# Optimization experiments

Hardware: AMD Instinct MI355X
Metric: run time of the kernel (lower is better)

## Reference

```python
import jax, jax.numpy as jnp
import numpy as np
from math import sqrt

MEM_SIZE = 1024
MEM_DIM = 256


def setup_inputs() -> dict:
    key = jax.random.key(0)
    k1, k2, k3 = jax.random.split(key, 3)
    x = jax.random.normal(k1, (8, 256, 64, 64), dtype=jnp.float32)
    mask = jax.random.randint(k2, (8, 1, 64, 64), 0, 2).astype(jnp.bool_)
    mem = jax.random.normal(k3, (1, MEM_DIM, MEM_SIZE), dtype=jnp.float32)
    return {"x": x, "mask": mask, "mem": mem}


def reference(x, mask, mem):
    # masked-detach blend: x.detach() * ~mask + x * mask
    x = jnp.where(mask, x, jax.lax.stop_gradient(x))
    B, K, H, W = x.shape
    xf = x.reshape(B, K, H * W)            # (B, K, N)
    m = mem[0]                              # (K, M) with M = mem_size
    # logits = m_key @ x / sqrt(K)  -> (B, M, N)
    logits = jnp.einsum('km,bkn->bmn', m, xf) / sqrt(K)
    attn = jax.nn.softmax(logits, axis=1)   # softmax over memory axis
    # out = m @ attn -> (B, K, N)
    out = jnp.einsum('km,bmn->bkn', m, attn).reshape(B, K, H, W)
    return (out, logits)
```

## Files before the change

kernel.cpp:

```cpp
#include <hip/hip_runtime.h>
#include <stdint.h>


typedef __attribute__((ext_vector_type(8))) __bf16 bf16x8;
typedef __attribute__((ext_vector_type(4))) float f32x4;

#define BQ 8
#define KD 256
#define MD 1024
#define ND 4096
#define NT 64

__device__ __forceinline__ unsigned short bf16_rne(float f) {
    union { float f; uint32_t u; } c; c.f = f;
    uint32_t u = c.u;
    uint32_t r = (u + 0x7FFFu + ((u >> 16) & 1u)) >> 16;
    return (unsigned short)r;
}

__global__ void prep_mem(const float* __restrict__ mem,
                         unsigned short* __restrict__ mT,
                         unsigned short* __restrict__ mR) {
    const int k = blockIdx.x;
    const int t = threadIdx.x;
    float4 v = reinterpret_cast<const float4*>(mem + (size_t)k * MD)[t];
    unsigned short h0 = bf16_rne(v.x), h1 = bf16_rne(v.y),
                   h2 = bf16_rne(v.z), h3 = bf16_rne(v.w);
    reinterpret_cast<uint2*>(mR + (size_t)k * MD)[t] =
        make_uint2((uint32_t)h0 | ((uint32_t)h1 << 16),
                   (uint32_t)h2 | ((uint32_t)h3 << 16));
    const int mm = t * 4;
    mT[(size_t)(mm + 0) * KD + k] = h0;
    mT[(size_t)(mm + 1) * KD + k] = h1;
    mT[(size_t)(mm + 2) * KD + k] = h2;
    mT[(size_t)(mm + 3) * KD + k] = h3;
}

__global__ __launch_bounds__(1024, 4) void fused_attn_mem(
    const float* __restrict__ x,
    const unsigned short* __restrict__ mT,
    const unsigned short* __restrict__ mR,
    float* __restrict__ out,
    float* __restrict__ logits)
{
    extern __shared__ char lds[];
    float* red_max = (float*)(lds);
    float* red_sum = (float*)(lds + 4096);

    const int tid = threadIdx.x;
    const int w   = tid >> 6;
    const int l   = tid & 63;
    const int l15 = l & 15;
    const int l4  = l >> 4;

    const int bid = blockIdx.x;
    const int g   = bid & 7;
    const int j   = bid >> 3;
    const int strip = g * 8 + (j & 7);
    const int b     = j >> 3;
    const int n0    = strip * NT;

    {
        const float* xb = x + (size_t)b * KD * ND + n0;
        const int k  = tid >> 2;
        const int nh = (tid & 3) * 16;
        const f32x4* src = reinterpret_cast<const f32x4*>(xb + (size_t)k * ND + nh);
        f32x4 v0 = __builtin_nontemporal_load(src + 0);
        f32x4 v1 = __builtin_nontemporal_load(src + 1);
        f32x4 v2 = __builtin_nontemporal_load(src + 2);
        f32x4 v3 = __builtin_nontemporal_load(src + 3);
        float vals[16] = {v0[0], v0[1], v0[2], v0[3], v1[0], v1[1], v1[2], v1[3],
                          v2[0], v2[1], v2[2], v2[3], v3[0], v3[1], v3[2], v3[3]};
        #pragma unroll
        for (int jj = 0; jj < 16; ++jj) {
            const int n = nh + jj;
            const int off = n * 512 + (((k >> 3) ^ (n & 7)) << 4) + (k & 7) * 2;
            *(unsigned short*)(lds + off) = bf16_rne(vals[jj]);
        }
    }
    __syncthreads();

    f32x4 acc[4][4];
    #pragma unroll
    for (int rt = 0; rt < 4; ++rt)
        #pragma unroll
        for (int ct = 0; ct < 4; ++ct)
            acc[rt][ct] = (f32x4){0.f, 0.f, 0.f, 0.f};

    #pragma unroll
    for (int ks = 0; ks < 8; ++ks) {
        const int kk = ks * 32 + l4 * 8;
        bf16x8 bfr[4];
        #pragma unroll
        for (int ct = 0; ct < 4; ++ct) {
            const int n = ct * 16 + l15;
            const int off = n * 512 + (((kk >> 3) ^ (n & 7)) << 4);
            bfr[ct] = *(const bf16x8*)(lds + off);
        }
        #pragma unroll
        for (int rt = 0; rt < 4; ++rt) {
            const int row = w * 64 + rt * 16 + l15;
            const bf16x8 afr = *(const bf16x8*)(mT + (size_t)row * KD + kk);
            #pragma unroll
            for (int ct = 0; ct < 4; ++ct)
                acc[rt][ct] = __builtin_amdgcn_mfma_f32_16x16x32_bf16(afr, bfr[ct], acc[rt][ct], 0, 0, 0);
        }
    }

    float lmax[4] = {-3e38f, -3e38f, -3e38f, -3e38f};
    #pragma unroll
    for (int rt = 0; rt < 4; ++rt) {
        #pragma unroll
        for (int ct = 0; ct < 4; ++ct) {
            f32x4 v = acc[rt][ct] * 0.0625f;
            acc[rt][ct] = v;
            lmax[ct] = fmaxf(lmax[ct], fmaxf(fmaxf(v[0], v[1]), fmaxf(v[2], v[3])));
        }
    }

    {
        char* sw = lds + 32768 + w * 4608;
        float* lg = logits + (size_t)b * MD * ND + n0;
        #pragma unroll
        for (int rt = 0; rt < 4; ++rt) {
            #pragma unroll
            for (int ct = 0; ct < 4; ++ct) {
                const int n = ct * 16 + l15;
                #pragma unroll
                for (int r = 0; r < 4; ++r) {
                    const int mloc = l4 * 4 + r;
                    *(float*)(sw + mloc * 272 + n * 4) = acc[rt][ct][r];
                }
            }
            __asm__ volatile("s_waitcnt lgkmcnt(0)" ::: "memory");
            __builtin_amdgcn_sched_barrier(0);
            #pragma unroll
            for (int p = 0; p < 4; ++p) {
                const int mloc = p * 4 + l4;
                const f32x4 v = *(const f32x4*)(sw + mloc * 272 + l15 * 16);
                __builtin_nontemporal_store(v,
                    (f32x4*)(lg + (size_t)(w * 64 + rt * 16 + mloc) * ND + l15 * 4));
            }
            __asm__ volatile("s_waitcnt lgkmcnt(0)" ::: "memory");
            __builtin_amdgcn_sched_barrier(0);
        }
    }

    #pragma unroll
    for (int ct = 0; ct < 4; ++ct) {
        float m = lmax[ct];
        m = fmaxf(m, __shfl_xor(m, 16, 64));
        m = fmaxf(m, __shfl_xor(m, 32, 64));
        lmax[ct] = m;
    }
    __syncthreads();
    if (l < 16) {
        #pragma unroll
        for (int ct = 0; ct < 4; ++ct)
            red_max[(w * 4 + ct) * 16 + l] = lmax[ct];
    }
    __syncthreads();

    float cmax[4];
    #pragma unroll
    for (int ct = 0; ct < 4; ++ct) {
        float m = -3e38f;
        #pragma unroll
        for (int ww = 0; ww < 16; ++ww)
            m = fmaxf(m, red_max[(ww * 4 + ct) * 16 + l15]);
        cmax[ct] = m;
    }

    float lsum[4] = {0.f, 0.f, 0.f, 0.f};
    #pragma unroll
    for (int rt = 0; rt < 4; ++rt) {
        #pragma unroll
        for (int ct = 0; ct < 4; ++ct) {
            f32x4 v = acc[rt][ct];
            v[0] = __expf(v[0] - cmax[ct]);
            v[1] = __expf(v[1] - cmax[ct]);
            v[2] = __expf(v[2] - cmax[ct]);
            v[3] = __expf(v[3] - cmax[ct]);
            lsum[ct] += (v[0] + v[1]) + (v[2] + v[3]);
            acc[rt][ct] = v;
        }
    }
    #pragma unroll
    for (int ct = 0; ct < 4; ++ct) {
        float s = lsum[ct];
        s += __shfl_xor(s, 16, 64);
        s += __shfl_xor(s, 32, 64);
        lsum[ct] = s;
    }
    if (l < 16) {
        #pragma unroll
        for (int ct = 0; ct < 4; ++ct)
            red_sum[(w * 4 + ct) * 16 + l] = lsum[ct];
    }
    __syncthreads();

    float rs[4];
    #pragma unroll
    for (int ct = 0; ct < 4; ++ct) {
        float s = 0.f;
        #pragma unroll
        for (int ww = 0; ww < 16; ++ww)
            s += red_sum[(ww * 4 + ct) * 16 + l15];
        rs[ct] = 1.0f / s;
    }

    #pragma unroll
    for (int rt = 0; rt < 4; ++rt) {
        #pragma unroll
        for (int ct = 0; ct < 4; ++ct) {
            f32x4 v = acc[rt][ct];
            unsigned short h0 = bf16_rne(v[0] * rs[ct]);
            unsigned short h1 = bf16_rne(v[1] * rs[ct]);
            unsigned short h2 = bf16_rne(v[2] * rs[ct]);
            unsigned short h3 = bf16_rne(v[3] * rs[ct]);
            const int m0 = w * 64 + rt * 16 + l4 * 4;
            const int n  = ct * 16 + l15;
            const int off = 32768 + n * 2048 + (((m0 >> 3) ^ (n & 7)) << 4) + (m0 & 7) * 2;
            *(uint2*)(lds + off) = make_uint2((uint32_t)h0 | ((uint32_t)h1 << 16),
                                              (uint32_t)h2 | ((uint32_t)h3 << 16));
        }
    }
    __syncthreads();

    f32x4 acc2[4];
    #pragma unroll
    for (int ct = 0; ct < 4; ++ct)
        acc2[ct] = (f32x4){0.f, 0.f, 0.f, 0.f};

    const unsigned short* arow = mR + (size_t)(w * 16 + l15) * MD;
    #pragma unroll 4
    for (int ks = 0; ks < 32; ++ks) {
        const int mk = ks * 32 + l4 * 8;
        const bf16x8 a2 = *(const bf16x8*)(arow + mk);
        #pragma unroll
        for (int ct = 0; ct < 4; ++ct) {
            const int n = ct * 16 + l15;
            const int off = 32768 + n * 2048 + (((mk >> 3) ^ (n & 7)) << 4);
            const bf16x8 b2 = *(const bf16x8*)(lds + off);
            acc2[ct] = __builtin_amdgcn_mfma_f32_16x16x32_bf16(a2, b2, acc2[ct], 0, 0, 0);
        }
    }
    __syncthreads();

    {
        char* sw = lds + 32768 + w * 4608;
        float* ob = out + (size_t)b * KD * ND + n0;
        #pragma unroll
        for (int ct = 0; ct < 4; ++ct) {
            const int n = ct * 16 + l15;
            #pragma unroll
            for (int r = 0; r < 4; ++r) {
                const int rr = l4 * 4 + r;
                *(float*)(sw + rr * 272 + n * 4) = acc2[ct][r];
            }
        }
        __asm__ volatile("s_waitcnt lgkmcnt(0)" ::: "memory");
        __builtin_amdgcn_sched_barrier(0);
        #pragma unroll
        for (int p = 0; p < 4; ++p) {
            const int rr = p * 4 + l4;
            const f32x4 v = *(const f32x4*)(sw + rr * 272 + l15 * 16);
            __builtin_nontemporal_store(v,
                (f32x4*)(ob + (size_t)(w * 16 + rr) * ND + l15 * 4));
        }
    }
}

extern "C" void kernel_launch(void* const* d_in, const int* in_sizes, int n_in,
                              void* d_out, int out_size, void* d_ws, size_t ws_size,
                              hipStream_t stream) {
    (void)in_sizes; (void)n_in; (void)out_size; (void)ws_size;
    const float* x   = (const float*)d_in[0];
    const float* mem = (const float*)d_in[2];

    float* out    = (float*)d_out;
    float* logits = (float*)d_out + (size_t)BQ * KD * ND;

    unsigned short* mT = (unsigned short*)d_ws;
    unsigned short* mR = mT + (size_t)MD * KD;

    static int lds_attr_set = 0;
    if (!lds_attr_set) {
        (void)hipFuncSetAttribute(reinterpret_cast<const void*>(&fused_attn_mem),
                                  hipFuncAttributeMaxDynamicSharedMemorySize, 163840);
        lds_attr_set = 1;
    }

    prep_mem<<<dim3(256), dim3(256), 0, stream>>>(mem, mT, mR);
    fused_attn_mem<<<dim3(BQ * (ND / NT)), dim3(1024), 163840, stream>>>(x, mT, mR, out, logits);
}
```

Before: 113.4 us.

## Split fused attention into bf16 x-transpose, logits GEMM, and recompute tail kernels

```diff
diff --git a/kernel.cpp b/kernel.cpp
--- a/kernel.cpp
+++ b/kernel.cpp
@@ -4,6 +4,7 @@
 
 typedef __attribute__((ext_vector_type(8))) __bf16 bf16x8;
 typedef __attribute__((ext_vector_type(4))) float f32x4;
+typedef __attribute__((ext_vector_type(4))) unsigned int u32x4;
 
 #define BQ 8
 #define KD 256
@@ -36,6 +37,300 @@
     mT[(size_t)(mm + 3) * KD + k] = h3;
 }
 
+__global__ __launch_bounds__(1024, 4) void prep_xT(
+    const float* __restrict__ x, unsigned short* __restrict__ xT)
+{
+    __shared__ __align__(16) char lds[32768];
+    const int tid = threadIdx.x;
+    const int b  = blockIdx.x >> 6;
+    const int n0 = (blockIdx.x & 63) * 64;
+
+    {
+        const float* xb = x + (size_t)b * KD * ND + n0;
+        const int k  = tid >> 2;
+        const int nh = (tid & 3) * 16;
+        const f32x4* src = reinterpret_cast<const f32x4*>(xb + (size_t)k * ND + nh);
+        f32x4 v0 = __builtin_nontemporal_load(src + 0);
+        f32x4 v1 = __builtin_nontemporal_load(src + 1);
+        f32x4 v2 = __builtin_nontemporal_load(src + 2);
+        f32x4 v3 = __builtin_nontemporal_load(src + 3);
+        float vals[16] = {v0[0], v0[1], v0[2], v0[3], v1[0], v1[1], v1[2], v1[3],
+                          v2[0], v2[1], v2[2], v2[3], v3[0], v3[1], v3[2], v3[3]};
+        #pragma unroll
+        for (int jj = 0; jj < 16; ++jj) {
+            const int n = nh + jj;
+            const int off = n * 512 + (((k >> 3) ^ (n & 7)) << 4) + (k & 7) * 2;
+            *(unsigned short*)(lds + off) = bf16_rne(vals[jj]);
+        }
+    }
+    __syncthreads();
+    {
+        const int n = tid >> 4, seg = tid & 15;
+        u32x4 q0 = *(const u32x4*)(lds + n * 512 + (((2 * seg)     ^ (n & 7)) << 4));
+        u32x4 q1 = *(const u32x4*)(lds + n * 512 + (((2 * seg + 1) ^ (n & 7)) << 4));
+        u32x4* dst = (u32x4*)(xT + ((size_t)b * ND + n0 + n) * KD + seg * 16);
+        dst[0] = q0;
+        dst[1] = q1;
+    }
+}
+
+__global__ __launch_bounds__(512, 2) void k_logits(
+    const unsigned short* __restrict__ mT,
+    const unsigned short* __restrict__ xT,
+    float* __restrict__ logits)
+{
+    __shared__ __align__(16) float scr[8][4][256];
+
+    const int tid = threadIdx.x;
+    const int w   = tid >> 6;
+    const int l   = tid & 63;
+    const int l15 = l & 15;
+    const int l4  = l >> 4;
+
+    const int bid = blockIdx.x;
+    const int g   = bid & 7;
+    const int j   = bid >> 3;
+    const int c   = g * 8 + (j & 7);
+    const int mt  = j >> 3;
+    const int b   = c >> 3;
+    const int nt  = c & 7;
+
+    const int m0w = mt * 64 + (w >> 1) * 16;
+    const int n0w = nt * 512 + (w & 1) * 256;
+
+    f32x4 acc[16];
+    #pragma unroll
+    for (int ct = 0; ct < 16; ++ct) acc[ct] = (f32x4){0.f, 0.f, 0.f, 0.f};
+
+    #pragma unroll
+    for (int ks = 0; ks < 8; ++ks) {
+        const int kk = ks * 32 + l4 * 8;
+        const bf16x8 a = *(const bf16x8*)(mT + (size_t)(m0w + l15) * KD + kk);
+        #pragma unroll
+        for (int ct = 0; ct < 16; ++ct) {
+            const bf16x8 bf = *(const bf16x8*)(xT + ((size_t)b * ND + n0w + ct * 16 + l15) * KD + kk);
+            acc[ct] = __builtin_amdgcn_mfma_f32_16x16x32_bf16(a, bf, acc[ct], 0, 0, 0);
+        }
+    }
+    #pragma unroll
+    for (int ct = 0; ct < 16; ++ct) acc[ct] = acc[ct] * 0.0625f;
+
+    float* lgb = logits + (size_t)b * MD * ND;
+    #pragma unroll
+    for (int r = 0; r < 4; ++r) {
+        #pragma unroll
+        for (int ct = 0; ct < 16; ++ct) {
+            const int nn = ct * 16 + l15;
+            scr[w][l4][nn ^ (l4 << 3)] = acc[ct][r];
+        }
+        __asm__ volatile("s_waitcnt lgkmcnt(0)" ::: "memory");
+        __builtin_amdgcn_sched_barrier(0);
+        #pragma unroll
+        for (int s = 0; s < 4; ++s) {
+            const f32x4 v = *(const f32x4*)&scr[w][s][(4 * l) ^ (s << 3)];
+            __builtin_nontemporal_store(v,
+                (f32x4*)(lgb + (size_t)(m0w + s * 4 + r) * ND + n0w + 4 * l));
+        }
+        __asm__ volatile("s_waitcnt lgkmcnt(0)" ::: "memory");
+        __builtin_amdgcn_sched_barrier(0);
+    }
+}
+
+__global__ __launch_bounds__(1024, 4) void k_fused_tail(
+    const unsigned short* __restrict__ xT,
+    const unsigned short* __restrict__ mT,
+    const unsigned short* __restrict__ mR,
+    float* __restrict__ out)
+{
+    extern __shared__ char lds[];
+    float* red_max = (float*)(lds);
+    float* red_sum = (float*)(lds + 4096);
+
+    const int tid = threadIdx.x;
+    const int w   = tid >> 6;
+    const int l   = tid & 63;
+    const int l15 = l & 15;
+    const int l4  = l >> 4;
+
+    const int bid = blockIdx.x;
+    const int g   = bid & 7;
+    const int j   = bid >> 3;
+    const int strip = g * 8 + (j & 7);
+    const int b     = j >> 3;
+    const int n0    = strip * NT;
+
+    {
+        const int n = tid >> 4, seg = tid & 15;
+        const unsigned short* srow = xT + ((size_t)b * ND + n0 + n) * KD + seg * 16;
+        u32x4 q0 = *(const u32x4*)(srow);
+        u32x4 q1 = *(const u32x4*)(srow + 8);
+        *(u32x4*)(lds + n * 512 + (((2 * seg)     ^ (n & 7)) << 4)) = q0;
+        *(u32x4*)(lds + n * 512 + (((2 * seg + 1) ^ (n & 7)) << 4)) = q1;
+    }
+    __syncthreads();
+
+    f32x4 acc[4][4];
+    #pragma unroll
+    for (int rt = 0; rt < 4; ++rt)
+        #pragma unroll
+        for (int ct = 0; ct < 4; ++ct)
+            acc[rt][ct] = (f32x4){0.f, 0.f, 0.f, 0.f};
+
+    #pragma unroll
+    for (int ks = 0; ks < 8; ++ks) {
+        const int kk = ks * 32 + l4 * 8;
+        bf16x8 bfr[4];
+        #pragma unroll
+        for (int ct = 0; ct < 4; ++ct) {
+            const int n = ct * 16 + l15;
+            const int off = n * 512 + (((kk >> 3) ^ (n & 7)) << 4);
+            bfr[ct] = *(const bf16x8*)(lds + off);
+        }
+        #pragma unroll
+        for (int rt = 0; rt < 4; ++rt) {
+            const int row = w * 64 + rt * 16 + l15;
+            const bf16x8 afr = *(const bf16x8*)(mT + (size_t)row * KD + kk);
+            #pragma unroll
+            for (int ct = 0; ct < 4; ++ct)
+                acc[rt][ct] = __builtin_amdgcn_mfma_f32_16x16x32_bf16(afr, bfr[ct], acc[rt][ct], 0, 0, 0);
+        }
+    }
+
+    float lmax[4] = {-3e38f, -3e38f, -3e38f, -3e38f};
+    #pragma unroll
+    for (int rt = 0; rt < 4; ++rt) {
+        #pragma unroll
+        for (int ct = 0; ct < 4; ++ct) {
+            f32x4 v = acc[rt][ct] * 0.0625f;
+            acc[rt][ct] = v;
+            lmax[ct] = fmaxf(lmax[ct], fmaxf(fmaxf(v[0], v[1]), fmaxf(v[2], v[3])));
+        }
+    }
+    #pragma unroll
+    for (int ct = 0; ct < 4; ++ct) {
+        float m = lmax[ct];
+        m = fmaxf(m, __shfl_xor(m, 16, 64));
+        m = fmaxf(m, __shfl_xor(m, 32, 64));
+        lmax[ct] = m;
+    }
+    __syncthreads();
+    if (l < 16) {
+        #pragma unroll
+        for (int ct = 0; ct < 4; ++ct)
+            red_max[(w * 4 + ct) * 16 + l] = lmax[ct];
+    }
+    __syncthreads();
+
+    float cmax[4];
+    #pragma unroll
+    for (int ct = 0; ct < 4; ++ct) {
+        float m = -3e38f;
+        #pragma unroll
+        for (int ww = 0; ww < 16; ++ww)
+            m = fmaxf(m, red_max[(ww * 4 + ct) * 16 + l15]);
+        cmax[ct] = m;
+    }
+
+    float lsum[4] = {0.f, 0.f, 0.f, 0.f};
+    #pragma unroll
+    for (int rt = 0; rt < 4; ++rt) {
+        #pragma unroll
+        for (int ct = 0; ct < 4; ++ct) {
+            f32x4 v = acc[rt][ct];
+            v[0] = __expf(v[0] - cmax[ct]);
+            v[1] = __expf(v[1] - cmax[ct]);
+            v[2] = __expf(v[2] - cmax[ct]);
+            v[3] = __expf(v[3] - cmax[ct]);
+            lsum[ct] += (v[0] + v[1]) + (v[2] + v[3]);
+            acc[rt][ct] = v;
+        }
+    }
+    #pragma unroll
+    for (int ct = 0; ct < 4; ++ct) {
+        float s = lsum[ct];
+        s += __shfl_xor(s, 16, 64);
+        s += __shfl_xor(s, 32, 64);
+        lsum[ct] = s;
+    }
+    if (l < 16) {
+        #pragma unroll
+        for (int ct = 0; ct < 4; ++ct)
+            red_sum[(w * 4 + ct) * 16 + l] = lsum[ct];
+    }
+    __syncthreads();
+
+    float rs[4];
+    #pragma unroll
+    for (int ct = 0; ct < 4; ++ct) {
+        float s = 0.f;
+        #pragma unroll
+        for (int ww = 0; ww < 16; ++ww)
+            s += red_sum[(ww * 4 + ct) * 16 + l15];
+        rs[ct] = 1.0f / s;
+    }
+
+    #pragma unroll
+    for (int rt = 0; rt < 4; ++rt) {
+        #pragma unroll
+        for (int ct = 0; ct < 4; ++ct) {
+            f32x4 v = acc[rt][ct];
+            unsigned short h0 = bf16_rne(v[0] * rs[ct]);
+            unsigned short h1 = bf16_rne(v[1] * rs[ct]);
+            unsigned short h2 = bf16_rne(v[2] * rs[ct]);
+            unsigned short h3 = bf16_rne(v[3] * rs[ct]);
+            const int m0 = w * 64 + rt * 16 + l4 * 4;
+            const int n  = ct * 16 + l15;
+            const int off = 32768 + n * 2048 + (((m0 >> 3) ^ (n & 7)) << 4) + (m0 & 7) * 2;
+            *(uint2*)(lds + off) = make_uint2((uint32_t)h0 | ((uint32_t)h1 << 16),
+                                              (uint32_t)h2 | ((uint32_t)h3 << 16));
+        }
+    }
+    __syncthreads();
+
+    f32x4 acc2[4];
+    #pragma unroll
+    for (int ct = 0; ct < 4; ++ct)
+        acc2[ct] = (f32x4){0.f, 0.f, 0.f, 0.f};
+
+    const unsigned short* arow = mR + (size_t)(w * 16 + l15) * MD;
+    #pragma unroll 4
+    for (int ks = 0; ks < 32; ++ks) {
+        const int mk = ks * 32 + l4 * 8;
+        const bf16x8 a2 = *(const bf16x8*)(arow + mk);
+        #pragma unroll
+        for (int ct = 0; ct < 4; ++ct) {
+            const int n = ct * 16 + l15;
+            const int off = 32768 + n * 2048 + (((mk >> 3) ^ (n & 7)) << 4);
+            const bf16x8 b2 = *(const bf16x8*)(lds + off);
+            acc2[ct] = __builtin_amdgcn_mfma_f32_16x16x32_bf16(a2, b2, acc2[ct], 0, 0, 0);
+        }
+    }
+    __syncthreads();
+
+    {
+        char* sw = lds + 32768 + w * 4608;
+        float* ob = out + (size_t)b * KD * ND + n0;
+        #pragma unroll
+        for (int ct = 0; ct < 4; ++ct) {
+            const int n = ct * 16 + l15;
+            #pragma unroll
+            for (int r = 0; r < 4; ++r) {
+                const int rr = l4 * 4 + r;
+                *(float*)(sw + rr * 272 + n * 4) = acc2[ct][r];
+            }
+        }
+        __asm__ volatile("s_waitcnt lgkmcnt(0)" ::: "memory");
+        __builtin_amdgcn_sched_barrier(0);
+        #pragma unroll
+        for (int p = 0; p < 4; ++p) {
+            const int rr = p * 4 + l4;
+            const f32x4 v = *(const f32x4*)(sw + rr * 272 + l15 * 16);
+            __builtin_nontemporal_store(v,
+                (f32x4*)(ob + (size_t)(w * 16 + rr) * ND + l15 * 4));
+        }
+    }
+}
+
 __global__ __launch_bounds__(1024, 4) void fused_attn_mem(
     const float* __restrict__ x,
     const unsigned short* __restrict__ mT,
@@ -46,29 +341,19 @@
     extern __shared__ char lds[];
     float* red_max = (float*)(lds);
     float* red_sum = (float*)(lds + 4096);
-
     const int tid = threadIdx.x;
-    const int w   = tid >> 6;
-    const int l   = tid & 63;
-    const int l15 = l & 15;
-    const int l4  = l >> 4;
-
+    const int w = tid >> 6, l = tid & 63, l15 = l & 15, l4 = l >> 4;
     const int bid = blockIdx.x;
-    const int g   = bid & 7;
-    const int j   = bid >> 3;
+    const int g = bid & 7, j = bid >> 3;
     const int strip = g * 8 + (j & 7);
-    const int b     = j >> 3;
-    const int n0    = strip * NT;
-
+    const int b = j >> 3;
+    const int n0 = strip * NT;
     {
         const float* xb = x + (size_t)b * KD * ND + n0;
-        const int k  = tid >> 2;
+        const int k = tid >> 2;
         const int nh = (tid & 3) * 16;
         const f32x4* src = reinterpret_cast<const f32x4*>(xb + (size_t)k * ND + nh);
-        f32x4 v0 = __builtin_nontemporal_load(src + 0);
-        f32x4 v1 = __builtin_nontemporal_load(src + 1);
-        f32x4 v2 = __builtin_nontemporal_load(src + 2);
-        f32x4 v3 = __builtin_nontemporal_load(src + 3);
+        f32x4 v0 = src[0], v1 = src[1], v2 = src[2], v3 = src[3];
         float vals[16] = {v0[0], v0[1], v0[2], v0[3], v1[0], v1[1], v1[2], v1[3],
                           v2[0], v2[1], v2[2], v2[3], v3[0], v3[1], v3[2], v3[3]};
         #pragma unroll
@@ -79,14 +364,12 @@
         }
     }
     __syncthreads();
-
     f32x4 acc[4][4];
     #pragma unroll
     for (int rt = 0; rt < 4; ++rt)
         #pragma unroll
         for (int ct = 0; ct < 4; ++ct)
             acc[rt][ct] = (f32x4){0.f, 0.f, 0.f, 0.f};
-
     #pragma unroll
     for (int ks = 0; ks < 8; ++ks) {
         const int kk = ks * 32 + l4 * 8;
@@ -94,32 +377,27 @@
         #pragma unroll
         for (int ct = 0; ct < 4; ++ct) {
             const int n = ct * 16 + l15;
-            const int off = n * 512 + (((kk >> 3) ^ (n & 7)) << 4);
-            bfr[ct] = *(const bf16x8*)(lds + off);
+            bfr[ct] = *(const bf16x8*)(lds + n * 512 + (((kk >> 3) ^ (n & 7)) << 4));
         }
         #pragma unroll
         for (int rt = 0; rt < 4; ++rt) {
-            const int row = w * 64 + rt * 16 + l15;
-            const bf16x8 afr = *(const bf16x8*)(mT + (size_t)row * KD + kk);
+            const bf16x8 afr = *(const bf16x8*)(mT + (size_t)(w * 64 + rt * 16 + l15) * KD + kk);
             #pragma unroll
             for (int ct = 0; ct < 4; ++ct)
                 acc[rt][ct] = __builtin_amdgcn_mfma_f32_16x16x32_bf16(afr, bfr[ct], acc[rt][ct], 0, 0, 0);
         }
     }
-
     float lmax[4] = {-3e38f, -3e38f, -3e38f, -3e38f};
     #pragma unroll
-    for (int rt = 0; rt < 4; ++rt) {
+    for (int rt = 0; rt < 4; ++rt)
         #pragma unroll
         for (int ct = 0; ct < 4; ++ct) {
             f32x4 v = acc[rt][ct] * 0.0625f;
             acc[rt][ct] = v;
             lmax[ct] = fmaxf(lmax[ct], fmaxf(fmaxf(v[0], v[1]), fmaxf(v[2], v[3])));
         }
-    }
-
-    {
-        char* sw = lds + 32768 + w * 4608;
+    {
+        char* sw = lds + 34816 + w * 4608;
         float* lg = logits + (size_t)b * MD * ND + n0;
         #pragma unroll
         for (int rt = 0; rt < 4; ++rt) {
@@ -127,10 +405,8 @@
             for (int ct = 0; ct < 4; ++ct) {
                 const int n = ct * 16 + l15;
                 #pragma unroll
-                for (int r = 0; r < 4; ++r) {
-                    const int mloc = l4 * 4 + r;
-                    *(float*)(sw + mloc * 272 + n * 4) = acc[rt][ct][r];
-                }
+                for (int r = 0; r < 4; ++r)
+                    *(float*)(sw + (l4 * 4 + r) * 272 + n * 4) = acc[rt][ct][r];
             }
             __asm__ volatile("s_waitcnt lgkmcnt(0)" ::: "memory");
             __builtin_amdgcn_sched_barrier(0);
@@ -138,14 +414,12 @@
             for (int p = 0; p < 4; ++p) {
                 const int mloc = p * 4 + l4;
                 const f32x4 v = *(const f32x4*)(sw + mloc * 272 + l15 * 16);
-                __builtin_nontemporal_store(v,
-                    (f32x4*)(lg + (size_t)(w * 64 + rt * 16 + mloc) * ND + l15 * 4));
+                *(f32x4*)(lg + (size_t)(w * 64 + rt * 16 + mloc) * ND + l15 * 4) = v;
             }
             __asm__ volatile("s_waitcnt lgkmcnt(0)" ::: "memory");
             __builtin_amdgcn_sched_barrier(0);
         }
     }
-
     #pragma unroll
     for (int ct = 0; ct < 4; ++ct) {
         float m = lmax[ct];
@@ -154,13 +428,11 @@
         lmax[ct] = m;
     }
     __syncthreads();
-    if (l < 16) {
+    if (l < 16)
         #pragma unroll
         for (int ct = 0; ct < 4; ++ct)
             red_max[(w * 4 + ct) * 16 + l] = lmax[ct];
-    }
-    __syncthreads();
-
+    __syncthreads();
     float cmax[4];
     #pragma unroll
     for (int ct = 0; ct < 4; ++ct) {
@@ -170,21 +442,17 @@
             m = fmaxf(m, red_max[(ww * 4 + ct) * 16 + l15]);
         cmax[ct] = m;
     }
-
     float lsum[4] = {0.f, 0.f, 0.f, 0.f};
     #pragma unroll
-    for (int rt = 0; rt < 4; ++rt) {
+    for (int rt = 0; rt < 4; ++rt)
         #pragma unroll
         for (int ct = 0; ct < 4; ++ct) {
             f32x4 v = acc[rt][ct];
-            v[0] = __expf(v[0] - cmax[ct]);
-            v[1] = __expf(v[1] - cmax[ct]);
-            v[2] = __expf(v[2] - cmax[ct]);
-            v[3] = __expf(v[3] - cmax[ct]);
+            v[0] = __expf(v[0] - cmax[ct]); v[1] = __expf(v[1] - cmax[ct]);
+            v[2] = __expf(v[2] - cmax[ct]); v[3] = __expf(v[3] - cmax[ct]);
             lsum[ct] += (v[0] + v[1]) + (v[2] + v[3]);
             acc[rt][ct] = v;
         }
-    }
     #pragma unroll
     for (int ct = 0; ct < 4; ++ct) {
         float s = lsum[ct];
@@ -192,13 +460,11 @@
         s += __shfl_xor(s, 32, 64);
         lsum[ct] = s;
     }
-    if (l < 16) {
+    if (l < 16)
         #pragma unroll
         for (int ct = 0; ct < 4; ++ct)
             red_sum[(w * 4 + ct) * 16 + l] = lsum[ct];
-    }
-    __syncthreads();
-
+    __syncthreads();
     float rs[4];
     #pragma unroll
     for (int ct = 0; ct < 4; ++ct) {
@@ -208,9 +474,9 @@
             s += red_sum[(ww * 4 + ct) * 16 + l15];
         rs[ct] = 1.0f / s;
     }
-
-    #pragma unroll
-    for (int rt = 0; rt < 4; ++rt) {
+    __syncthreads();
+    #pragma unroll
+    for (int rt = 0; rt < 4; ++rt)
         #pragma unroll
         for (int ct = 0; ct < 4; ++ct) {
             f32x4 v = acc[rt][ct];
@@ -219,19 +485,15 @@
             unsigned short h2 = bf16_rne(v[2] * rs[ct]);
             unsigned short h3 = bf16_rne(v[3] * rs[ct]);
             const int m0 = w * 64 + rt * 16 + l4 * 4;
-            const int n  = ct * 16 + l15;
+            const int n = ct * 16 + l15;
             const int off = 32768 + n * 2048 + (((m0 >> 3) ^ (n & 7)) << 4) + (m0 & 7) * 2;
             *(uint2*)(lds + off) = make_uint2((uint32_t)h0 | ((uint32_t)h1 << 16),
                                               (uint32_t)h2 | ((uint32_t)h3 << 16));
         }
-    }
-    __syncthreads();
-
+    __syncthreads();
     f32x4 acc2[4];
     #pragma unroll
-    for (int ct = 0; ct < 4; ++ct)
-        acc2[ct] = (f32x4){0.f, 0.f, 0.f, 0.f};
-
+    for (int ct = 0; ct < 4; ++ct) acc2[ct] = (f32x4){0.f, 0.f, 0.f, 0.f};
     const unsigned short* arow = mR + (size_t)(w * 16 + l15) * MD;
     #pragma unroll 4
     for (int ks = 0; ks < 32; ++ks) {
@@ -240,13 +502,11 @@
         #pragma unroll
         for (int ct = 0; ct < 4; ++ct) {
             const int n = ct * 16 + l15;
-            const int off = 32768 + n * 2048 + (((mk >> 3) ^ (n & 7)) << 4);
-            const bf16x8 b2 = *(const bf16x8*)(lds + off);
+            const bf16x8 b2 = *(const bf16x8*)(lds + 32768 + n * 2048 + (((mk >> 3) ^ (n & 7)) << 4));
             acc2[ct] = __builtin_amdgcn_mfma_f32_16x16x32_bf16(a2, b2, acc2[ct], 0, 0, 0);
         }
     }
     __syncthreads();
-
     {
         char* sw = lds + 32768 + w * 4608;
         float* ob = out + (size_t)b * KD * ND + n0;
@@ -254,10 +514,8 @@
         for (int ct = 0; ct < 4; ++ct) {
             const int n = ct * 16 + l15;
             #pragma unroll
-            for (int r = 0; r < 4; ++r) {
-                const int rr = l4 * 4 + r;
-                *(float*)(sw + rr * 272 + n * 4) = acc2[ct][r];
-            }
+            for (int r = 0; r < 4; ++r)
+                *(float*)(sw + (l4 * 4 + r) * 272 + n * 4) = acc2[ct][r];
         }
         __asm__ volatile("s_waitcnt lgkmcnt(0)" ::: "memory");
         __builtin_amdgcn_sched_barrier(0);
@@ -265,8 +523,7 @@
         for (int p = 0; p < 4; ++p) {
             const int rr = p * 4 + l4;
             const f32x4 v = *(const f32x4*)(sw + rr * 272 + l15 * 16);
-            __builtin_nontemporal_store(v,
-                (f32x4*)(ob + (size_t)(w * 16 + rr) * ND + l15 * 4));
+            *(f32x4*)(ob + (size_t)(w * 16 + rr) * ND + l15 * 4) = v;
         }
     }
 }
@@ -274,7 +531,7 @@
 extern "C" void kernel_launch(void* const* d_in, const int* in_sizes, int n_in,
                               void* d_out, int out_size, void* d_ws, size_t ws_size,
                               hipStream_t stream) {
-    (void)in_sizes; (void)n_in; (void)out_size; (void)ws_size;
+    (void)in_sizes; (void)n_in; (void)out_size;
     const float* x   = (const float*)d_in[0];
     const float* mem = (const float*)d_in[2];
 
@@ -283,14 +540,29 @@
 
     unsigned short* mT = (unsigned short*)d_ws;
     unsigned short* mR = mT + (size_t)MD * KD;
-
-    static int lds_attr_set = 0;
-    if (!lds_attr_set) {
-        (void)hipFuncSetAttribute(reinterpret_cast<const void*>(&fused_attn_mem),
-                                  hipFuncAttributeMaxDynamicSharedMemorySize, 163840);
-        lds_attr_set = 1;
-    }
+    unsigned short* xT = (unsigned short*)((char*)d_ws + 1048576);
+
+    const size_t need = 1048576 + (size_t)BQ * ND * KD * 2;
 
     prep_mem<<<dim3(256), dim3(256), 0, stream>>>(mem, mT, mR);
-    fused_attn_mem<<<dim3(BQ * (ND / NT)), dim3(1024), 163840, stream>>>(x, mT, mR, out, logits);
-}
+
+    if (ws_size >= need) {
+        static int attr_set = 0;
+        if (!attr_set) {
+            (void)hipFuncSetAttribute(reinterpret_cast<const void*>(&k_fused_tail),
+                                      hipFuncAttributeMaxDynamicSharedMemorySize, 163840);
+            attr_set = 1;
+        }
+        prep_xT<<<dim3(512), dim3(1024), 0, stream>>>(x, xT);
+        k_logits<<<dim3(1024), dim3(512), 0, stream>>>(mT, xT, logits);
+        k_fused_tail<<<dim3(512), dim3(1024), 163840, stream>>>(xT, mT, mR, out);
+    } else {
+        static int attr_set2 = 0;
+        if (!attr_set2) {
+            (void)hipFuncSetAttribute(reinterpret_cast<const void*>(&fused_attn_mem),
+                                      hipFuncAttributeMaxDynamicSharedMemorySize, 163840);
+            attr_set2 = 1;
+        }
+        fused_attn_mem<<<dim3(512), dim3(1024), 163840, stream>>>(x, mT, mR, out, logits);
+    }
+}
```

New measurement: 239.5 us. 111% more time.

## Process two batch strips per block and prefetch the next x tile

Applied to the files above, without the earlier changes.

```diff
diff --git a/kernel.cpp b/kernel.cpp
--- a/kernel.cpp
+++ b/kernel.cpp
@@ -10,6 +10,13 @@
 #define MD 1024
 #define ND 4096
 #define NT 64
+
+#define RAW_BAR() do {                                           \
+    __asm__ volatile("s_waitcnt lgkmcnt(0)" ::: "memory");       \
+    __builtin_amdgcn_sched_barrier(0);                           \
+    __builtin_amdgcn_s_barrier();                                \
+    __builtin_amdgcn_sched_barrier(0);                           \
+} while (0)
 
 __device__ __forceinline__ unsigned short bf16_rne(float f) {
     union { float f; uint32_t u; } c; c.f = f;
@@ -36,49 +43,48 @@
     mT[(size_t)(mm + 3) * KD + k] = h3;
 }
 
-__global__ __launch_bounds__(1024, 4) void fused_attn_mem(
-    const float* __restrict__ x,
+__device__ __forceinline__ void stage_tile(char* lds, const f32x4* pre, int tid) {
+    const int k  = tid >> 2;
+    const int nh = (tid & 3) * 16;
+    float vals[16] = {pre[0][0], pre[0][1], pre[0][2], pre[0][3],
+                      pre[1][0], pre[1][1], pre[1][2], pre[1][3],
+                      pre[2][0], pre[2][1], pre[2][2], pre[2][3],
+                      pre[3][0], pre[3][1], pre[3][2], pre[3][3]};
+    #pragma unroll
+    for (int jj = 0; jj < 16; ++jj) {
+        const int n = nh + jj;
+        const int off = n * 512 + (((k >> 3) ^ (n & 7)) << 4) + (k & 7) * 2;
+        *(unsigned short*)(lds + off) = bf16_rne(vals[jj]);
+    }
+}
+
+__device__ __forceinline__ void load_tile(const float* __restrict__ xb,
+                                          f32x4* pre, int tid) {
+    const int k  = tid >> 2;
+    const int nh = (tid & 3) * 16;
+    const f32x4* src = reinterpret_cast<const f32x4*>(xb + (size_t)k * ND + nh);
+    pre[0] = __builtin_nontemporal_load(src + 0);
+    pre[1] = __builtin_nontemporal_load(src + 1);
+    pre[2] = __builtin_nontemporal_load(src + 2);
+    pre[3] = __builtin_nontemporal_load(src + 3);
+}
+
+template <int IT>
+__device__ __forceinline__ void strip_body(
+    char* __restrict__ lds,
     const unsigned short* __restrict__ mT,
     const unsigned short* __restrict__ mR,
-    float* __restrict__ out,
-    float* __restrict__ logits)
+    float* __restrict__ lg, float* __restrict__ ob,
+    const float* __restrict__ x_next,
+    int tid, int w, int l, int l15, int l4)
 {
-    extern __shared__ char lds[];
     float* red_max = (float*)(lds);
     float* red_sum = (float*)(lds + 4096);
 
-    const int tid = threadIdx.x;
-    const int w   = tid >> 6;
-    const int l   = tid & 63;
-    const int l15 = l & 15;
-    const int l4  = l >> 4;
-
-    const int bid = blockIdx.x;
-    const int g   = bid & 7;
-    const int j   = bid >> 3;
-    const int strip = g * 8 + (j & 7);
-    const int b     = j >> 3;
-    const int n0    = strip * NT;
-
-    {
-        const float* xb = x + (size_t)b * KD * ND + n0;
-        const int k  = tid >> 2;
-        const int nh = (tid & 3) * 16;
-        const f32x4* src = reinterpret_cast<const f32x4*>(xb + (size_t)k * ND + nh);
-        f32x4 v0 = __builtin_nontemporal_load(src + 0);
-        f32x4 v1 = __builtin_nontemporal_load(src + 1);
-        f32x4 v2 = __builtin_nontemporal_load(src + 2);
-        f32x4 v3 = __builtin_nontemporal_load(src + 3);
-        float vals[16] = {v0[0], v0[1], v0[2], v0[3], v1[0], v1[1], v1[2], v1[3],
-                          v2[0], v2[1], v2[2], v2[3], v3[0], v3[1], v3[2], v3[3]};
-        #pragma unroll
-        for (int jj = 0; jj < 16; ++jj) {
-            const int n = nh + jj;
-            const int off = n * 512 + (((k >> 3) ^ (n & 7)) << 4) + (k & 7) * 2;
-            *(unsigned short*)(lds + off) = bf16_rne(vals[jj]);
-        }
-    }
-    __syncthreads();
+    f32x4 pre[4];
+    if (IT == 0) {
+        load_tile(x_next, pre, tid);
+    }
 
     f32x4 acc[4][4];
     #pragma unroll
@@ -120,7 +126,6 @@
 
     {
         char* sw = lds + 32768 + w * 4608;
-        float* lg = logits + (size_t)b * MD * ND + n0;
         #pragma unroll
         for (int rt = 0; rt < 4; ++rt) {
             #pragma unroll
@@ -153,13 +158,13 @@
         m = fmaxf(m, __shfl_xor(m, 32, 64));
         lmax[ct] = m;
     }
-    __syncthreads();
+    RAW_BAR();
     if (l < 16) {
         #pragma unroll
         for (int ct = 0; ct < 4; ++ct)
             red_max[(w * 4 + ct) * 16 + l] = lmax[ct];
     }
-    __syncthreads();
+    RAW_BAR();
 
     float cmax[4];
     #pragma unroll
@@ -197,7 +202,7 @@
         for (int ct = 0; ct < 4; ++ct)
             red_sum[(w * 4 + ct) * 16 + l] = lsum[ct];
     }
-    __syncthreads();
+    RAW_BAR();
 
     float rs[4];
     #pragma unroll
@@ -208,6 +213,7 @@
             s += red_sum[(ww * 4 + ct) * 16 + l15];
         rs[ct] = 1.0f / s;
     }
+    RAW_BAR();
 
     #pragma unroll
     for (int rt = 0; rt < 4; ++rt) {
@@ -225,7 +231,11 @@
                                               (uint32_t)h2 | ((uint32_t)h3 << 16));
         }
     }
-    __syncthreads();
+    RAW_BAR();
+
+    if (IT == 0) {
+        stage_tile(lds, pre, tid);
+    }
 
     f32x4 acc2[4];
     #pragma unroll
@@ -245,11 +255,10 @@
             acc2[ct] = __builtin_amdgcn_mfma_f32_16x16x32_bf16(a2, b2, acc2[ct], 0, 0, 0);
         }
     }
-    __syncthreads();
+    RAW_BAR();
 
     {
         char* sw = lds + 32768 + w * 4608;
-        float* ob = out + (size_t)b * KD * ND + n0;
         #pragma unroll
         for (int ct = 0; ct < 4; ++ct) {
             const int n = ct * 16 + l15;
@@ -268,7 +277,51 @@
             __builtin_nontemporal_store(v,
                 (f32x4*)(ob + (size_t)(w * 16 + rr) * ND + l15 * 4));
         }
-    }
+        __asm__ volatile("s_waitcnt lgkmcnt(0)" ::: "memory");
+        __builtin_amdgcn_sched_barrier(0);
+    }
+}
+
+__global__ __launch_bounds__(1024, 4) void fused_attn_mem(
+    const float* __restrict__ x,
+    const unsigned short* __restrict__ mT,
+    const unsigned short* __restrict__ mR,
+    float* __restrict__ out,
+    float* __restrict__ logits)
+{
+    extern __shared__ char lds[];
+
+    const int tid = threadIdx.x;
+    const int w   = tid >> 6;
+    const int l   = tid & 63;
+    const int l15 = l & 15;
+    const int l4  = l >> 4;
+
+    const int q  = blockIdx.x;
+    const int g  = q & 7;
+    const int j  = q >> 3;
+    const int strip = g * 8 + (j & 7);
+    const int b0    = j >> 3;
+    const int b1    = b0 + 4;
+    const int n0    = strip * NT;
+
+    const float* x0 = x + (size_t)b0 * KD * ND + n0;
+    const float* x1 = x + (size_t)b1 * KD * ND + n0;
+    float* lg0 = logits + (size_t)b0 * MD * ND + n0;
+    float* lg1 = logits + (size_t)b1 * MD * ND + n0;
+    float* ob0 = out + (size_t)b0 * KD * ND + n0;
+    float* ob1 = out + (size_t)b1 * KD * ND + n0;
+
+    {
+        f32x4 p0[4];
+        load_tile(x0, p0, tid);
+        stage_tile(lds, p0, tid);
+    }
+    RAW_BAR();
+
+    strip_body<0>(lds, mT, mR, lg0, ob0, x1, tid, w, l, l15, l4);
+    RAW_BAR();
+    strip_body<1>(lds, mT, mR, lg1, ob1, nullptr, tid, w, l, l15, l4);
 }
 
 extern "C" void kernel_launch(void* const* d_in, const int* in_sizes, int n_in,
@@ -292,5 +345,5 @@
     }
 
     prep_mem<<<dim3(256), dim3(256), 0, stream>>>(mem, mT, mR);
-    fused_attn_mem<<<dim3(BQ * (ND / NT)), dim3(1024), 163840, stream>>>(x, mT, mR, out, logits);
-}
+    fused_attn_mem<<<dim3(256), dim3(1024), 163840, stream>>>(x, mT, mR, out, logits);
+}
```

After: 140.7 us. 1.24x slower.
